# Optimization experiments

Measured on AMD Instinct MI355X. Metric: run time of the kernel, lower is better.

The kernel has to match this reference:

```python
import jax, jax.numpy as jnp
from jax import lax
import numpy as np

N, F_IN, D_MODEL = 8192, 128, 256
D_INNER, D_STATE, D_CONV, DT_RANK = 512, 16, 4, 16  # expand=2, d_state=16, d_conv=4, dt_rank=ceil(256/16)
BN_EPS = 1e-5


def setup_inputs() -> dict:
    key = jax.random.key(0)
    ks = jax.random.split(key, 12)
    rn = lambda k, s, sc: jax.random.normal(k, s, jnp.float32) * sc
    x = rn(ks[0], (N, F_IN), 1.0)
    # normalized dense adjacency (row sums ~1)
    adj = jax.random.uniform(ks[1], (N, N), jnp.float32) * (2.0 / N)
    w_gcn = rn(ks[2], (F_IN, D_MODEL), 1.0 / np.sqrt(F_IN))
    b_gcn = rn(ks[3], (D_MODEL,), 0.02)
    bn_gamma = jnp.ones((D_MODEL,), jnp.float32)
    bn_beta = jnp.zeros((D_MODEL,), jnp.float32)
    w_in = rn(ks[4], (2 * D_INNER, D_MODEL), 1.0 / np.sqrt(D_MODEL))
    conv_w = rn(ks[5], (D_INNER, D_CONV), 1.0 / np.sqrt(D_CONV))
    conv_b = rn(ks[6], (D_INNER,), 0.02)
    w_xproj = rn(ks[7], (DT_RANK + 2 * D_STATE, D_INNER), 1.0 / np.sqrt(D_INNER))
    w_dt = rn(ks[8], (D_INNER, DT_RANK), 1.0 / np.sqrt(DT_RANK))
    b_dt = rn(ks[9], (D_INNER,), 0.1)
    A_log = jnp.log(jnp.broadcast_to(jnp.arange(1, D_STATE + 1, dtype=jnp.float32), (D_INNER, D_STATE)))
    D_skip = jnp.ones((D_INNER,), jnp.float32)
    w_out = rn(ks[10], (D_MODEL, D_INNER), 1.0 / np.sqrt(D_INNER))
    return dict(x=x, adj=adj, w_gcn=w_gcn, b_gcn=b_gcn, bn_gamma=bn_gamma, bn_beta=bn_beta,
                w_in=w_in, conv_w=conv_w, conv_b=conv_b, w_xproj=w_xproj, w_dt=w_dt,
                b_dt=b_dt, A_log=A_log, D_skip=D_skip, w_out=w_out)


def _forward(x, adj, w_gcn, b_gcn, bn_gamma, bn_beta, w_in, conv_w, conv_b,
             w_xproj, w_dt, b_dt, A_log, D_skip, w_out):
    # --- GCN layer: adj @ (x @ W) + b ---
    h = adj @ (x @ w_gcn) + b_gcn            # (N, D_MODEL)
    h = jax.nn.relu(h)
    # dropout: eval mode -> identity
    # --- BatchNorm1d (batch statistics, biased var, as torch training norm) ---
    mean = jnp.mean(h, axis=0)
    var = jnp.var(h, axis=0)
    h = (h - mean) * lax.rsqrt(var + BN_EPS) * bn_gamma + bn_beta  # (N, D_MODEL)

    # --- Mamba block, batch=1, seq_len=N ---
    xz = h @ w_in.T                          # (N, 2*D_INNER)
    xm, z = jnp.split(xz, 2, axis=-1)        # (N, D_INNER) each

    # causal depthwise conv1d (kernel D_CONV) + SiLU
    xp = jnp.pad(xm, ((D_CONV - 1, 0), (0, 0)))
    xc = conv_b + sum(xp[i:i + N] * conv_w[:, i] for i in range(D_CONV))  # (N, D_INNER)
    xc = jax.nn.silu(xc)

    # input-dependent SSM parameters
    x_dbl = xc @ w_xproj.T                   # (N, DT_RANK + 2*D_STATE)
    dt_r = x_dbl[:, :DT_RANK]
    B = x_dbl[:, DT_RANK:DT_RANK + D_STATE]  # (N, D_STATE)
    C = x_dbl[:, DT_RANK + D_STATE:]         # (N, D_STATE)
    dt = jax.nn.softplus(dt_r @ w_dt.T + b_dt)  # (N, D_INNER)

    A = -jnp.exp(A_log)                      # (D_INNER, D_STATE)
    deltaA = jnp.exp(dt[:, :, None] * A[None])                 # (N, D_INNER, D_STATE)
    deltaBu = dt[:, :, None] * B[:, None, :] * xc[:, :, None]  # (N, D_INNER, D_STATE)

    def step(hs, inp):
        dA, dBu, c = inp
        hs = dA * hs + dBu                   # (D_INNER, D_STATE)
        return hs, hs @ c                    # emit (D_INNER,)

    h0 = jnp.zeros((D_INNER, D_STATE), xc.dtype)
    _, ys = lax.scan(step, h0, (deltaA, deltaBu, C))  # ys: (N, D_INNER)

    y = ys + D_skip * xc
    y = y * jax.nn.silu(z)
    out_m = y @ w_out.T                      # (N, D_MODEL)
    return out_m + h                         # residual


def reference(x, adj, w_gcn, b_gcn, bn_gamma, bn_beta, w_in, conv_w, conv_b,
              w_xproj, w_dt, b_dt, A_log, D_skip, w_out):
    return _forward(x, adj, w_gcn, b_gcn, bn_gamma, bn_beta, w_in, conv_w, conv_b,
                    w_xproj, w_dt, b_dt, A_log, D_skip, w_out)
```

## Files before the change

kernel.cpp:

```cpp
#include <hip/hip_runtime.h>
#include <stdint.h>

#define NN   8192
#define FIN  128
#define DM   256
#define DI   512
#define DST  16
#define NC   256
#define CL   32

typedef short bf16x8 __attribute__((ext_vector_type(8)));
typedef float f32x4 __attribute__((ext_vector_type(4)));
union FragU { unsigned u[4]; uint4 u4; bf16x8 v; };

__device__ __forceinline__ unsigned short f2bf(float x){
  unsigned u = __float_as_uint(x);
  return (unsigned short)((u + 0x7FFFu + ((u >> 16) & 1u)) >> 16);
}
__device__ __forceinline__ unsigned pack2(float a, float b){
  return (unsigned)f2bf(a) | ((unsigned)f2bf(b) << 16);
}
__device__ __forceinline__ unsigned pack2rn(float a, float b){
  unsigned ua = __float_as_uint(a) + 0x8000u;
  unsigned ub = __float_as_uint(b) + 0x8000u;
  return __builtin_amdgcn_perm(ub, ua, 0x07060302u);
}
__device__ __forceinline__ float bf2f(unsigned short u){
  return __uint_as_float(((unsigned)u) << 16);
}
__device__ __forceinline__ float sigmoidf_(float x){ return 1.f / (1.f + __expf(-x)); }
__device__ __forceinline__ f32x4 zero4(){ f32x4 z; z[0]=0.f; z[1]=0.f; z[2]=0.f; z[3]=0.f; return z; }

#define ASYNC16(g, l) __builtin_amdgcn_global_load_lds( \
    (const __attribute__((address_space(1))) void*)(g), \
    (__attribute__((address_space(3))) void*)(l), 16, 0, 0)
#define WAITVM3  asm volatile("s_waitcnt vmcnt(3)" ::: "memory")
#define WAITVM0  asm volatile("s_waitcnt vmcnt(0)" ::: "memory")
#define WAITLGKM0 asm volatile("s_waitcnt lgkmcnt(0)" ::: "memory")
#define BARRIER  asm volatile("s_barrier" ::: "memory")

constexpr size_t OFF_XWT   = 0;
constexpr size_t OFF_HP    = OFF_XWT   + (size_t)DM*NN*2;
constexpr size_t OFF_HB    = OFF_HP    + (size_t)2*NN*DM*4;
constexpr size_t OFF_HBNB  = OFF_HB    + (size_t)NN*DM*2;
constexpr size_t OFF_WINB  = OFF_HBNB  + (size_t)NN*DM*2;
constexpr size_t OFF_WXPB  = OFF_WINB  + (size_t)1024*256*2;
constexpr size_t OFF_WOUTB = OFF_WXPB  + (size_t)48*512*2;
constexpr size_t OFF_XMB   = OFF_WOUTB + (size_t)256*512*2;
constexpr size_t OFF_ZB    = OFF_XMB   + (size_t)NN*DI*2;
constexpr size_t OFF_XC    = OFF_ZB    + (size_t)NN*DI*2;
constexpr size_t OFF_XCB   = OFF_XC    + (size_t)NN*DI*4;
constexpr size_t OFF_XDBL  = OFF_XCB   + (size_t)NN*DI*2;
constexpr size_t OFF_DT    = OFF_XDBL  + (size_t)NN*48*4;
constexpr size_t OFF_PF    = OFF_DT    + (size_t)NN*DI*4;
constexpr size_t OFF_CY    = OFF_PF    + (size_t)NC*DI*DST*8;
constexpr size_t OFF_YB    = OFF_CY    + (size_t)NC*DI*DST*4;
constexpr size_t OFF_BNS   = OFF_YB    + (size_t)NN*DI*2;
constexpr size_t OFF_BNS2  = OFF_BNS   + 256*4;
constexpr size_t WS_NEED   = OFF_BNS2  + 256*4;

__global__ __launch_bounds__(256) void prep_kernel(
    const float* __restrict__ w_in, const float* __restrict__ w_xp, const float* __restrict__ w_out,
    unsigned short* __restrict__ o_in, unsigned short* __restrict__ o_xp, unsigned short* __restrict__ o_out)
{
  int i = blockIdx.x * 256 + threadIdx.x;
  if (i < 1024*256) o_in[i]  = f2bf(w_in[i]);
  if (i < 48*512)   o_xp[i]  = f2bf(w_xp[i]);
  if (i < 256*512)  o_out[i] = f2bf(w_out[i]);
}

__global__ __launch_bounds__(256) void gemm1_kernel(
    const float* __restrict__ x, const float* __restrict__ w, unsigned short* __restrict__ xwT)
{
  __shared__ float xs[16*128];
  const int t = threadIdx.x;
  const int m0 = blockIdx.x * 16;
  {
    int r = t >> 4, c0 = (t & 15) * 8;
    const float* src = x + (size_t)(m0 + r)*FIN + c0;
    *(float4*)&xs[r*128 + c0]     = *(const float4*)src;
    *(float4*)&xs[r*128 + c0 + 4] = *(const float4*)(src + 4);
  }
  __syncthreads();
  const int n = t;
  float acc[16];
  #pragma unroll
  for (int m = 0; m < 16; ++m) acc[m] = 0.f;
  for (int k = 0; k < 128; k += 4){
    float w0 = w[(size_t)k*DM + n];
    float w1 = w[(size_t)(k+1)*DM + n];
    float w2 = w[(size_t)(k+2)*DM + n];
    float w3 = w[(size_t)(k+3)*DM + n];
    #pragma unroll
    for (int m = 0; m < 16; ++m){
      float4 xv = *(const float4*)&xs[m*128 + k];
      acc[m] = fmaf(xv.x, w0, acc[m]);
      acc[m] = fmaf(xv.y, w1, acc[m]);
      acc[m] = fmaf(xv.z, w2, acc[m]);
      acc[m] = fmaf(xv.w, w3, acc[m]);
    }
  }
  unsigned outp[8];
  #pragma unroll
  for (int m = 0; m < 8; ++m) outp[m] = pack2(acc[2*m], acc[2*m+1]);
  unsigned short* dst = xwT + (size_t)n*NN + m0;
  ((uint4*)dst)[0] = *(uint4*)&outp[0];
  ((uint4*)dst)[1] = *(uint4*)&outp[4];
}

__global__ __launch_bounds__(512) void gemm2_kernel(
    const float* __restrict__ adj, const unsigned short* __restrict__ xwT,
    float* __restrict__ hp)
{
  __shared__ char lds[2][24576];
  const int t = threadIdx.x;
  const int wave = t >> 6, lane = t & 63, r = lane & 15, q = lane >> 4;
  const int mt = (int)blockIdx.x & 127, ks = (int)blockIdx.x >> 7;
  const int m0 = mt * 64;
  const int kb = ks * 4096;
  const int wm = wave & 1, wn = wave >> 1;

  const int arow = t >> 3;
  const int asg  = (t & 7) ^ (arow & 7);
  const float* asrc = adj + (size_t)(m0 + arow)*NN + kb + asg*4;
  const int adst = t * 16;
  const int bn0 = t >> 2;
  const int bs0 = (t & 3) ^ ((bn0 >> 1) & 3);
  const int bn1 = (512 + t) >> 2;
  const int bs1 = ((512 + t) & 3) ^ ((bn1 >> 1) & 3);
  const unsigned short* bsrc0 = xwT + (size_t)bn0*NN + kb + bs0*8;
  const unsigned short* bsrc1 = xwT + (size_t)bn1*NN + kb + bs1*8;
  const int bdst0 = 8192 + t*16;
  const int bdst1 = 8192 + (512 + t)*16;

  f32x4 acc[2][4];
  #pragma unroll
  for (int mi = 0; mi < 2; ++mi)
    #pragma unroll
    for (int ni = 0; ni < 4; ++ni) acc[mi][ni] = zero4();

  ASYNC16(asrc,       lds[0] + adst);
  ASYNC16(bsrc0,      lds[0] + bdst0);
  ASYNC16(bsrc1,      lds[0] + bdst1);
  ASYNC16(asrc + 32,  lds[1] + adst);
  ASYNC16(bsrc0 + 32, lds[1] + bdst0);
  ASYNC16(bsrc1 + 32, lds[1] + bdst1);

  const int ar0 = wm*32 + r;
  const int ar1 = ar0 + 16;
  const int aoff00 = ar0*32 + (((2*q)   ^ (ar0 & 7)) << 2);
  const int aoff01 = ar0*32 + (((2*q+1) ^ (ar0 & 7)) << 2);
  const int aoff10 = ar1*32 + (((2*q)   ^ (ar1 & 7)) << 2);
  const int aoff11 = ar1*32 + (((2*q+1) ^ (ar1 & 7)) << 2);
  int boff[4];
  #pragma unroll
  for (int ni = 0; ni < 4; ++ni){
    int nl = wn*64 + ni*16 + r;
    boff[ni] = nl*4 + (q ^ ((nl >> 1) & 3));
  }

  #pragma unroll 2
  for (int k = 0; k < 128; ++k){
    if (k < 127) { WAITVM3; } else { WAITVM0; }
    BARRIER;
    const float* Af = (const float*)lds[k & 1];
    const uint4* Bf = (const uint4*)(lds[k & 1] + 8192);
    float4 p00 = *(const float4*)(Af + aoff00);
    float4 p01 = *(const float4*)(Af + aoff01);
    float4 p10 = *(const float4*)(Af + aoff10);
    float4 p11 = *(const float4*)(Af + aoff11);
    FragU fb[4];
    #pragma unroll
    for (int ni = 0; ni < 4; ++ni) fb[ni].u4 = Bf[boff[ni]];
    WAITLGKM0;
    BARRIER;
    if (k + 2 < 128){
      int k0 = (k + 2) * 32;
      char* L = lds[k & 1];
      ASYNC16(asrc + k0,  L + adst);
      ASYNC16(bsrc0 + k0, L + bdst0);
      ASYNC16(bsrc1 + k0, L + bdst1);
    }
    FragU fa0, fa1;
    fa0.u[0] = pack2rn(p00.x, p00.y); fa0.u[1] = pack2rn(p00.z, p00.w);
    fa0.u[2] = pack2rn(p01.x, p01.y); fa0.u[3] = pack2rn(p01.z, p01.w);
    fa1.u[0] = pack2rn(p10.x, p10.y); fa1.u[1] = pack2rn(p10.z, p10.w);
    fa1.u[2] = pack2rn(p11.x, p11.y); fa1.u[3] = pack2rn(p11.z, p11.w);
    #pragma unroll
    for (int ni = 0; ni < 4; ++ni){
      acc[0][ni] = __builtin_amdgcn_mfma_f32_16x16x32_bf16(fa0.v, fb[ni].v, acc[0][ni], 0, 0, 0);
      acc[1][ni] = __builtin_amdgcn_mfma_f32_16x16x32_bf16(fa1.v, fb[ni].v, acc[1][ni], 0, 0, 0);
    }
  }

  float* hpo = hp + (size_t)ks * ((size_t)NN * DM);
  #pragma unroll
  for (int mi = 0; mi < 2; ++mi)
    #pragma unroll
    for (int ni = 0; ni < 4; ++ni){
      const int n = wn*64 + ni*16 + r;
      #pragma unroll
      for (int jr = 0; jr < 4; ++jr){
        const int m = m0 + wm*32 + mi*16 + q*4 + jr;
        hpo[(size_t)m*DM + n] = acc[mi][ni][jr];
      }
    }
}

__global__ __launch_bounds__(256) void hred_kernel(
    const float* __restrict__ hp, const float* __restrict__ b_gcn,
    unsigned short* __restrict__ hb, float* __restrict__ bns, float* __restrict__ bns2)
{
  const int c = threadIdx.x;
  const int m0 = blockIdx.x * 32;
  const float bias = b_gcn[c];
  float s1 = 0.f, s2 = 0.f;
  #pragma unroll 8
  for (int rr = 0; rr < 32; ++rr){
    size_t idx = (size_t)(m0 + rr)*DM + c;
    float v = hp[idx] + hp[(size_t)NN*DM + idx] + bias;
    v = fmaxf(v, 0.f);
    hb[idx] = f2bf(v);
    s1 += v; s2 += v*v;
  }
  atomicAdd(bns + c, s1);
  atomicAdd(bns2 + c, s2);
}

__global__ __launch_bounds__(256) void bnapply_kernel(
    const unsigned short* __restrict__ hb, const float* __restrict__ s1, const float* __restrict__ s2,
    const float* __restrict__ gamma, const float* __restrict__ beta,
    unsigned short* __restrict__ hbnb)
{
  int base = (blockIdx.x*256 + threadIdx.x) * 2;
  int c0 = base & (DM - 1);
  ushort2 hv = *(const ushort2*)(hb + base);
  float mA = s1[c0] * (1.f/NN),   mB = s1[c0+1] * (1.f/NN);
  float vA = s2[c0] * (1.f/NN) - mA*mA, vB = s2[c0+1] * (1.f/NN) - mB*mB;
  float iA = rsqrtf(vA + 1e-5f), iB = rsqrtf(vB + 1e-5f);
  float a = (bf2f(hv.x) - mA)*iA*gamma[c0]   + beta[c0];
  float b = (bf2f(hv.y) - mB)*iB*gamma[c0+1] + beta[c0+1];
  ushort2 o; o.x = f2bf(a); o.y = f2bf(b);
  *(ushort2*)(hbnb + base) = o;
}

__global__ __launch_bounds__(256) void gemm3_kernel(
    const unsigned short* __restrict__ Ab, const unsigned short* __restrict__ Wb,
    unsigned short* __restrict__ xmb, unsigned short* __restrict__ zb)
{
  __shared__ uint4 alds[2048];
  const int t = threadIdx.x;
  const int wave = t >> 6, lane = t & 63, r = lane & 15, q = lane >> 4;
  const int mb = ((int)blockIdx.x & 127) * 64;
  const int nb = ((int)blockIdx.x >> 7) * 128;
  const int wm = wave & 1, wn = wave >> 1;

  #pragma unroll
  for (int j = 0; j < 8; ++j){
    int si = j*256 + t;
    int row = si >> 5, dg = si & 31;
    int sg = dg ^ (row & 31);
    ASYNC16(Ab + (size_t)(mb + row)*DM + sg*8, (char*)alds + si*16);
  }
  __syncthreads();

  f32x4 acc[2][4];
  #pragma unroll
  for (int mi = 0; mi < 2; ++mi)
    #pragma unroll
    for (int ni = 0; ni < 4; ++ni) acc[mi][ni] = zero4();

  const unsigned short* bp[4];
  #pragma unroll
  for (int ni = 0; ni < 4; ++ni)
    bp[ni] = Wb + (size_t)(nb + wn*64 + ni*16 + r)*DM + q*8;
  FragU fb[4];
  #pragma unroll
  for (int ni = 0; ni < 4; ++ni) fb[ni].u4 = *(const uint4*)bp[ni];

  #pragma unroll
  for (int it = 0; it < 8; ++it){
    FragU fbn[4];
    if (it < 7){
      #pragma unroll
      for (int ni = 0; ni < 4; ++ni) fbn[ni].u4 = *(const uint4*)(bp[ni] + (it+1)*32);
    }
    FragU fa[2];
    #pragma unroll
    for (int mi = 0; mi < 2; ++mi){
      int row = wm*32 + mi*16 + r;
      int g = it*4 + q;
      fa[mi].u4 = alds[row*32 + (g ^ (row & 31))];
    }
    #pragma unroll
    for (int mi = 0; mi < 2; ++mi)
      #pragma unroll
      for (int ni = 0; ni < 4; ++ni)
        acc[mi][ni] = __builtin_amdgcn_mfma_f32_16x16x32_bf16(fa[mi].v, fb[ni].v, acc[mi][ni], 0, 0, 0);
    if (it < 7){
      #pragma unroll
      for (int ni = 0; ni < 4; ++ni) fb[ni] = fbn[ni];
    }
  }
  #pragma unroll
  for (int mi = 0; mi < 2; ++mi)
    #pragma unroll
    for (int ni = 0; ni < 4; ++ni){
      int nc = nb + wn*64 + ni*16 + r;
      unsigned short* dst = (nc < 512) ? (xmb + nc) : (zb + (nc - 512));
      #pragma unroll
      for (int jr = 0; jr < 4; ++jr){
        int m = mb + wm*32 + mi*16 + q*4 + jr;
        dst[(size_t)m*DI] = f2bf(acc[mi][ni][jr]);
      }
    }
}

__global__ __launch_bounds__(256) void conv_kernel(
    const unsigned short* __restrict__ xmb, const float* __restrict__ conv_w, const float* __restrict__ conv_b,
    float* __restrict__ xc, unsigned short* __restrict__ xcb)
{
  const int d0 = threadIdx.x * 2;
  const int n0 = blockIdx.x * 32;
  float4 wa = *(const float4*)(conv_w + (size_t)d0*4);
  float4 wb = *(const float4*)(conv_w + (size_t)d0*4 + 4);
  float2 bias = *(const float2*)(conv_b + d0);
  float x0a=0.f,x1a=0.f,x2a=0.f, x0b=0.f,x1b=0.f,x2b=0.f;
  #pragma unroll
  for (int j = 0; j < 3; ++j){
    int n = n0 - 3 + j;
    float va = 0.f, vb = 0.f;
    if (n >= 0){
      ushort2 u = *(const ushort2*)(xmb + (size_t)n*DI + d0);
      va = bf2f(u.x); vb = bf2f(u.y);
    }
    if (j == 0){ x0a = va; x0b = vb; }
    else if (j == 1){ x1a = va; x1b = vb; }
    else { x2a = va; x2b = vb; }
  }
  for (int j = 0; j < 32; ++j){
    int n = n0 + j;
    ushort2 u = *(const ushort2*)(xmb + (size_t)n*DI + d0);
    float x3a = bf2f(u.x), x3b = bf2f(u.y);
    float sa = bias.x + wa.x*x0a + wa.y*x1a + wa.z*x2a + wa.w*x3a;
    float sb = bias.y + wb.x*x0b + wb.y*x1b + wb.z*x2b + wb.w*x3b;
    float va = sa * sigmoidf_(sa);
    float vb = sb * sigmoidf_(sb);
    *(float2*)(xc + (size_t)n*DI + d0) = make_float2(va, vb);
    ushort2 o; o.x = f2bf(va); o.y = f2bf(vb);
    *(ushort2*)(xcb + (size_t)n*DI + d0) = o;
    x0a=x1a; x1a=x2a; x2a=x3a;
    x0b=x1b; x1b=x2b; x2b=x3b;
  }
}

__global__ __launch_bounds__(256) void gemm4_kernel(
    const unsigned short* __restrict__ Ab, const unsigned short* __restrict__ Wb, float* __restrict__ xdbl)
{
  __shared__ uint4 alds[2048];
  const int t = threadIdx.x;
  const int wave = t >> 6, lane = t & 63, r = lane & 15, q = lane >> 4;
  const int m0 = (int)blockIdx.x * 32;
  #pragma unroll
  for (int j = 0; j < 8; ++j){
    int si = j*256 + t;
    int row = si >> 6, dg = si & 63;
    int sg = dg ^ (row & 31);
    ASYNC16(Ab + (size_t)(m0 + row)*DI + sg*8, (char*)alds + si*16);
  }
  __syncthreads();
  f32x4 acc[2][3];
  #pragma unroll
  for (int mi = 0; mi < 2; ++mi)
    #pragma unroll
    for (int ni = 0; ni < 3; ++ni) acc[mi][ni] = zero4();
  const int kq = wave * 128;
  const unsigned short* bp[3];
  #pragma unroll
  for (int ni = 0; ni < 3; ++ni) bp[ni] = Wb + (size_t)(ni*16 + r)*DI + kq + q*8;
  FragU fb[3];
  #pragma unroll
  for (int ni = 0; ni < 3; ++ni) fb[ni].u4 = *(const uint4*)bp[ni];
  #pragma unroll
  for (int it = 0; it < 4; ++it){
    FragU fbn[3];
    if (it < 3){
      #pragma unroll
      for (int ni = 0; ni < 3; ++ni) fbn[ni].u4 = *(const uint4*)(bp[ni] + (it+1)*32);
    }
    FragU fa[2];
    #pragma unroll
    for (int mi = 0; mi < 2; ++mi){
      int row = mi*16 + r;
      int g = (kq >> 3) + it*4 + q;
      fa[mi].u4 = alds[row*64 + (g ^ (row & 31))];
    }
    #pragma unroll
    for (int mi = 0; mi < 2; ++mi)
      #pragma unroll
      for (int ni = 0; ni < 3; ++ni)
        acc[mi][ni] = __builtin_amdgcn_mfma_f32_16x16x32_bf16(fa[mi].v, fb[ni].v, acc[mi][ni], 0, 0, 0);
    if (it < 3){
      #pragma unroll
      for (int ni = 0; ni < 3; ++ni) fb[ni] = fbn[ni];
    }
  }
  __syncthreads();
  float* red = (float*)alds;
  if (wave > 0){
    int base = ((wave - 1)*64 + lane)*24;
    #pragma unroll
    for (int mi = 0; mi < 2; ++mi)
      #pragma unroll
      for (int ni = 0; ni < 3; ++ni)
        #pragma unroll
        for (int jr = 0; jr < 4; ++jr)
          red[base + (mi*3 + ni)*4 + jr] = acc[mi][ni][jr];
  }
  __syncthreads();
  if (wave == 0){
    #pragma unroll
    for (int w = 0; w < 3; ++w){
      int base = (w*64 + lane)*24;
      #pragma unroll
      for (int mi = 0; mi < 2; ++mi)
        #pragma unroll
        for (int ni = 0; ni < 3; ++ni)
          #pragma unroll
          for (int jr = 0; jr < 4; ++jr)
            acc[mi][ni][jr] += red[base + (mi*3 + ni)*4 + jr];
    }
    #pragma unroll
    for (int mi = 0; mi < 2; ++mi)
      #pragma unroll
      for (int ni = 0; ni < 3; ++ni)
        #pragma unroll
        for (int jr = 0; jr < 4; ++jr)
          xdbl[(size_t)(m0 + mi*16 + q*4 + jr)*48 + ni*16 + r] = acc[mi][ni][jr];
  }
}

__global__ __launch_bounds__(256) void dt_kernel(
    const float* __restrict__ xdbl, const float* __restrict__ w_dt, const float* __restrict__ b_dt,
    float* __restrict__ dt)
{
  __shared__ float xr[64*16];
  const int t = threadIdx.x;
  const int dg = (int)blockIdx.x & 1;
  const int n0 = ((int)blockIdx.x >> 1) * 64;
  const int d = dg*256 + t;
  #pragma unroll
  for (int j = 0; j < 4; ++j){
    int idx = t + 256*j;
    xr[idx] = xdbl[(size_t)(n0 + (idx >> 4))*48 + (idx & 15)];
  }
  __syncthreads();
  const float4* wp = (const float4*)(w_dt + (size_t)d*16);
  float4 w0 = wp[0], w1 = wp[1], w2 = wp[2], w3 = wp[3];
  float bias = b_dt[d];
  for (int j = 0; j < 64; ++j){
    const float4* xp = (const float4*)(xr + j*16);
    float4 a0 = xp[0], a1 = xp[1], a2 = xp[2], a3 = xp[3];
    float a = bias;
    a += w0.x*a0.x + w0.y*a0.y + w0.z*a0.z + w0.w*a0.w;
    a += w1.x*a1.x + w1.y*a1.y + w1.z*a1.z + w1.w*a1.w;
    a += w2.x*a2.x + w2.y*a2.y + w2.z*a2.z + w2.w*a2.w;
    a += w3.x*a3.x + w3.y*a3.y + w3.z*a3.z + w3.w*a3.w;
    float o = (a > 20.f) ? a : log1pf(__expf(a));
    dt[(size_t)(n0 + j)*DI + d] = o;
  }
}

__global__ __launch_bounds__(256) void scanA_kernel(
    const float* __restrict__ dt, const float* __restrict__ xc,
    const float* __restrict__ xdbl, const float* __restrict__ A_log,
    float2* __restrict__ PF)
{
  __shared__ float Bs[CL*DST];
  const int t = threadIdx.x;
  const int c = (int)blockIdx.x >> 1;
  const int d = (((int)blockIdx.x & 1) << 8) + t;
  #pragma unroll
  for (int j = 0; j < 2; ++j){
    int idx = t + 256*j;
    Bs[idx] = xdbl[(size_t)(c*CL + (idx >> 4))*48 + 16 + (idx & 15)];
  }
  __syncthreads();
  float Av[DST], hs[DST];
  {
    const float4* Ap = (const float4*)(A_log + (size_t)d*DST);
    #pragma unroll
    for (int s4 = 0; s4 < 4; ++s4){
      float4 a4 = Ap[s4];
      Av[s4*4+0] = -__expf(a4.x); Av[s4*4+1] = -__expf(a4.y);
      Av[s4*4+2] = -__expf(a4.z); Av[s4*4+3] = -__expf(a4.w);
    }
  }
  #pragma unroll
  for (int s = 0; s < DST; ++s) hs[s] = 0.f;
  float sdt = 0.f;
  const size_t rb = (size_t)c*CL*DI + d;
  float dtv = dt[rb], xcv = xc[rb];
  for (int tt = 0; tt < CL; ++tt){
    float dtn = 0.f, xcn = 0.f;
    if (tt + 1 < CL){
      dtn = dt[rb + (size_t)(tt+1)*DI];
      xcn = xc[rb + (size_t)(tt+1)*DI];
    }
    float u = dtv * xcv;
    sdt += dtv;
    float bv[DST];
    *(float4*)&bv[0]  = *(const float4*)&Bs[tt*16];
    *(float4*)&bv[4]  = *(const float4*)&Bs[tt*16 + 4];
    *(float4*)&bv[8]  = *(const float4*)&Bs[tt*16 + 8];
    *(float4*)&bv[12] = *(const float4*)&Bs[tt*16 + 12];
    #pragma unroll
    for (int s = 0; s < DST; ++s)
      hs[s] = __expf(dtv * Av[s]) * hs[s] + u * bv[s];
    dtv = dtn; xcv = xcn;
  }
  float4* out = (float4*)(PF + (size_t)c*(DI*DST) + (size_t)d*DST);
  #pragma unroll
  for (int j = 0; j < 8; ++j){
    float4 v;
    v.x = __expf(Av[2*j] * sdt);   v.y = hs[2*j];
    v.z = __expf(Av[2*j+1] * sdt); v.w = hs[2*j+1];
    out[j] = v;
  }
}

__global__ __launch_bounds__(128) void scanB_kernel(
    const float2* __restrict__ PF, float* __restrict__ Cy)
{
  const int ds = (int)blockIdx.x*128 + (int)threadIdx.x;
  float2 A0[16], A1[16];
  #pragma unroll
  for (int j = 0; j < 16; ++j) A0[j] = PF[(size_t)j*8192 + ds];
  #pragma unroll
  for (int j = 0; j < 16; ++j) A1[j] = PF[(size_t)(16 + j)*8192 + ds];
  float cy = 0.f;
  Cy[ds] = 0.f;
  #pragma unroll
  for (int g = 0; g < 16; ++g){
    #pragma unroll
    for (int j = 0; j < 16; ++j){
      int i = g*16 + j;
      if (i < NC - 1){
        float2 pf = (g & 1) ? A1[j] : A0[j];
        cy = pf.x * cy + pf.y;
        Cy[(size_t)(i + 1)*8192 + ds] = cy;
      }
    }
    int gn = g + 2;
    if (gn < 16){
      #pragma unroll
      for (int j = 0; j < 16; ++j){
        float2 v = PF[(size_t)(gn*16 + j)*8192 + ds];
        if (g & 1) A1[j] = v; else A0[j] = v;
      }
    }
  }
}

__global__ __launch_bounds__(256) void scanC_kernel(
    const float* __restrict__ dt, const float* __restrict__ xc,
    const float* __restrict__ xdbl, const float* __restrict__ A_log,
    const float* __restrict__ Cy, const float* __restrict__ Dskip,
    const unsigned short* __restrict__ zb, unsigned short* __restrict__ yb)
{
  __shared__ float Bs[CL*DST];
  __shared__ float Cs[CL*DST];
  const int t = threadIdx.x;
  const int c = (int)blockIdx.x >> 1;
  const int d = (((int)blockIdx.x & 1) << 8) + t;
  #pragma unroll
  for (int j = 0; j < 2; ++j){
    int idx = t + 256*j;
    int tg = c*CL + (idx >> 4);
    Bs[idx] = xdbl[(size_t)tg*48 + 16 + (idx & 15)];
    Cs[idx] = xdbl[(size_t)tg*48 + 32 + (idx & 15)];
  }
  __syncthreads();
  float Av[DST], hs[DST];
  {
    const float4* Ap = (const float4*)(A_log + (size_t)d*DST);
    #pragma unroll
    for (int s4 = 0; s4 < 4; ++s4){
      float4 a4 = Ap[s4];
      Av[s4*4+0] = -__expf(a4.x); Av[s4*4+1] = -__expf(a4.y);
      Av[s4*4+2] = -__expf(a4.z); Av[s4*4+3] = -__expf(a4.w);
    }
  }
  {
    const float4* hp4 = (const float4*)(Cy + (size_t)c*(DI*DST) + (size_t)d*DST);
    #pragma unroll
    for (int s4 = 0; s4 < 4; ++s4){
      float4 h4 = hp4[s4];
      hs[s4*4+0] = h4.x; hs[s4*4+1] = h4.y; hs[s4*4+2] = h4.z; hs[s4*4+3] = h4.w;
    }
  }
  const float Dv = Dskip[d];
  const size_t rb = (size_t)c*CL*DI + d;
  float dtv = dt[rb], xcv = xc[rb];
  unsigned short zv0 = zb[rb];
  for (int tt = 0; tt < CL; ++tt){
    float dtn = 0.f, xcn = 0.f;
    unsigned short zn = 0;
    if (tt + 1 < CL){
      dtn = dt[rb + (size_t)(tt+1)*DI];
      xcn = xc[rb + (size_t)(tt+1)*DI];
      zn  = zb[rb + (size_t)(tt+1)*DI];
    }
    float u = dtv * xcv;
    float bv[DST], cv[DST];
    *(float4*)&bv[0]  = *(const float4*)&Bs[tt*16];
    *(float4*)&bv[4]  = *(const float4*)&Bs[tt*16 + 4];
    *(float4*)&bv[8]  = *(const float4*)&Bs[tt*16 + 8];
    *(float4*)&bv[12] = *(const float4*)&Bs[tt*16 + 12];
    *(float4*)&cv[0]  = *(const float4*)&Cs[tt*16];
    *(float4*)&cv[4]  = *(const float4*)&Cs[tt*16 + 4];
    *(float4*)&cv[8]  = *(const float4*)&Cs[tt*16 + 8];
    *(float4*)&cv[12] = *(const float4*)&Cs[tt*16 + 12];
    float y0 = 0.f, y1 = 0.f;
    #pragma unroll
    for (int s = 0; s < DST; s += 2){
      hs[s]   = __expf(dtv * Av[s])   * hs[s]   + u * bv[s];
      hs[s+1] = __expf(dtv * Av[s+1]) * hs[s+1] + u * bv[s+1];
      y0 += hs[s]   * cv[s];
      y1 += hs[s+1] * cv[s+1];
    }
    float z = bf2f(zv0);
    float yf = ((y0 + y1) + Dv * xcv) * (z * sigmoidf_(z));
    yb[rb + (size_t)tt*DI] = f2bf(yf);
    dtv = dtn; xcv = xcn; zv0 = zn;
  }
}

__global__ __launch_bounds__(512) void gemm5_kernel(
    const unsigned short* __restrict__ yb, const unsigned short* __restrict__ Wb,
    const unsigned short* __restrict__ hbnb, float* __restrict__ out)
{
  __shared__ uint4 alds[2048];
  const int t = threadIdx.x;
  const int wave = t >> 6, lane = t & 63, r = lane & 15, q = lane >> 4;
  const int m0 = (int)blockIdx.x * 32;
  #pragma unroll
  for (int j = 0; j < 4; ++j){
    int si = j*512 + t;
    int row = si >> 6, dg = si & 63;
    int sg = dg ^ (row & 31);
    ASYNC16(yb + (size_t)(m0 + row)*DI + sg*8, (char*)alds + si*16);
  }
  __syncthreads();
  f32x4 acc[2][2];
  #pragma unroll
  for (int mi = 0; mi < 2; ++mi)
    #pragma unroll
    for (int ni = 0; ni < 2; ++ni) acc[mi][ni] = zero4();
  const int nw = wave * 32;
  const unsigned short* bp0 = Wb + (size_t)(nw + r)*DI + q*8;
  const unsigned short* bp1 = Wb + (size_t)(nw + 16 + r)*DI + q*8;
  FragU fb0, fb1;
  fb0.u4 = *(const uint4*)bp0;
  fb1.u4 = *(const uint4*)bp1;
  #pragma unroll
  for (int it = 0; it < 16; ++it){
    FragU fn0, fn1;
    if (it < 15){
      fn0.u4 = *(const uint4*)(bp0 + (it+1)*32);
      fn1.u4 = *(const uint4*)(bp1 + (it+1)*32);
    }
    FragU fa[2];
    #pragma unroll
    for (int mi = 0; mi < 2; ++mi){
      int row = mi*16 + r;
      int g = it*4 + q;
      fa[mi].u4 = alds[row*64 + (g ^ (row & 31))];
    }
    acc[0][0] = __builtin_amdgcn_mfma_f32_16x16x32_bf16(fa[0].v, fb0.v, acc[0][0], 0, 0, 0);
    acc[0][1] = __builtin_amdgcn_mfma_f32_16x16x32_bf16(fa[0].v, fb1.v, acc[0][1], 0, 0, 0);
    acc[1][0] = __builtin_amdgcn_mfma_f32_16x16x32_bf16(fa[1].v, fb0.v, acc[1][0], 0, 0, 0);
    acc[1][1] = __builtin_amdgcn_mfma_f32_16x16x32_bf16(fa[1].v, fb1.v, acc[1][1], 0, 0, 0);
    if (it < 15){ fb0 = fn0; fb1 = fn1; }
  }
  #pragma unroll
  for (int mi = 0; mi < 2; ++mi)
    #pragma unroll
    for (int ni = 0; ni < 2; ++ni){
      const int n = nw + ni*16 + r;
      #pragma unroll
      for (int jr = 0; jr < 4; ++jr){
        const int m = m0 + mi*16 + q*4 + jr;
        size_t idx = (size_t)m*DM + n;
        out[idx] = acc[mi][ni][jr] + bf2f(hbnb[idx]);
      }
    }
}

extern "C" void kernel_launch(void* const* d_in, const int* in_sizes, int n_in,
                              void* d_out, int out_size, void* d_ws, size_t ws_size,
                              hipStream_t stream)
{
  const float* x      = (const float*)d_in[0];
  const float* adj    = (const float*)d_in[1];
  const float* w_gcn  = (const float*)d_in[2];
  const float* b_gcn  = (const float*)d_in[3];
  const float* gamma  = (const float*)d_in[4];
  const float* beta   = (const float*)d_in[5];
  const float* w_in   = (const float*)d_in[6];
  const float* conv_w = (const float*)d_in[7];
  const float* conv_b = (const float*)d_in[8];
  const float* w_xp   = (const float*)d_in[9];
  const float* w_dt   = (const float*)d_in[10];
  const float* b_dt   = (const float*)d_in[11];
  const float* A_log  = (const float*)d_in[12];
  const float* D_skip = (const float*)d_in[13];
  const float* w_out  = (const float*)d_in[14];
  float* out = (float*)d_out;
  char* ws = (char*)d_ws;
  if (ws_size < WS_NEED) return;

  unsigned short* xwT   = (unsigned short*)(ws + OFF_XWT);
  float*          hp    = (float*)(ws + OFF_HP);
  unsigned short* hb    = (unsigned short*)(ws + OFF_HB);
  unsigned short* hbnb  = (unsigned short*)(ws + OFF_HBNB);
  unsigned short* winb  = (unsigned short*)(ws + OFF_WINB);
  unsigned short* wxpb  = (unsigned short*)(ws + OFF_WXPB);
  unsigned short* woutb = (unsigned short*)(ws + OFF_WOUTB);
  unsigned short* xmb   = (unsigned short*)(ws + OFF_XMB);
  unsigned short* zb    = (unsigned short*)(ws + OFF_ZB);
  float*          xc    = (float*)(ws + OFF_XC);
  unsigned short* xcb   = (unsigned short*)(ws + OFF_XCB);
  float*          xdbl  = (float*)(ws + OFF_XDBL);
  float*          dtb   = (float*)(ws + OFF_DT);
  float2*         PF    = (float2*)(ws + OFF_PF);
  float*          Cy    = (float*)(ws + OFF_CY);
  unsigned short* yb    = (unsigned short*)(ws + OFF_YB);
  float*          bns   = (float*)(ws + OFF_BNS);
  float*          bns2  = (float*)(ws + OFF_BNS2);

  hipMemsetAsync(bns, 0, 2*256*sizeof(float), stream);

  prep_kernel   <<<1024, 256, 0, stream>>>(w_in, w_xp, w_out, winb, wxpb, woutb);
  gemm1_kernel  <<<512,  256, 0, stream>>>(x, w_gcn, xwT);
  gemm2_kernel  <<<256,  512, 0, stream>>>(adj, xwT, hp);
  hred_kernel   <<<256,  256, 0, stream>>>(hp, b_gcn, hb, bns, bns2);
  bnapply_kernel<<<4096, 256, 0, stream>>>(hb, bns, bns2, gamma, beta, hbnb);
  gemm3_kernel  <<<1024, 256, 0, stream>>>(hbnb, winb, xmb, zb);
  conv_kernel   <<<256,  256, 0, stream>>>(xmb, conv_w, conv_b, xc, xcb);
  gemm4_kernel  <<<256,  256, 0, stream>>>(xcb, wxpb, xdbl);
  dt_kernel     <<<256,  256, 0, stream>>>(xdbl, w_dt, b_dt, dtb);
  scanA_kernel  <<<512,  256, 0, stream>>>(dtb, xc, xdbl, A_log, PF);
  scanB_kernel  <<<64,   128, 0, stream>>>(PF, Cy);
  scanC_kernel  <<<512,  256, 0, stream>>>(dtb, xc, xdbl, A_log, Cy, D_skip, zb, yb);
  gemm5_kernel  <<<256,  512, 0, stream>>>(yb, woutb, hbnb, out);
}
```

Measured before the change: 629.8 us.

## Enlarge adjacency GEMM tile to 128 rows with triple-buffered LDS pipeline

Doubles the M tile of the adj@xW GEMM from 64 to 128 rows per block. To keep the block count the same, split-K goes from 2 to 4 ways. The LDS pipeline moves from double to triple buffering with dynamic shared memory, so loads are issued three stages ahead. Each wave now computes 4x4 MFMA tiles, which reuses each B fragment across twice as many A rows. The partial-sum buffer is aliased onto the later PF scratch region, and the reduction kernel now sums four partials. The intent is to raise arithmetic intensity and latency hiding in the dominant GEMM. The cost is more registers, extra partial-sum traffic, and one block per CU.

New measurement: 598.0 us. -5.0%, faster.

```diff
diff --git a/kernel.cpp b/kernel.cpp
--- a/kernel.cpp
+++ b/kernel.cpp
@@ -34,14 +34,15 @@
 #define ASYNC16(g, l) __builtin_amdgcn_global_load_lds( \
     (const __attribute__((address_space(1))) void*)(g), \
     (__attribute__((address_space(3))) void*)(l), 16, 0, 0)
+#define WAITVM8  asm volatile("s_waitcnt vmcnt(8)" ::: "memory")
+#define WAITVM4  asm volatile("s_waitcnt vmcnt(4)" ::: "memory")
 #define WAITVM3  asm volatile("s_waitcnt vmcnt(3)" ::: "memory")
 #define WAITVM0  asm volatile("s_waitcnt vmcnt(0)" ::: "memory")
 #define WAITLGKM0 asm volatile("s_waitcnt lgkmcnt(0)" ::: "memory")
 #define BARRIER  asm volatile("s_barrier" ::: "memory")
 
 constexpr size_t OFF_XWT   = 0;
-constexpr size_t OFF_HP    = OFF_XWT   + (size_t)DM*NN*2;
-constexpr size_t OFF_HB    = OFF_HP    + (size_t)2*NN*DM*4;
+constexpr size_t OFF_HB    = OFF_XWT   + (size_t)DM*NN*2;
 constexpr size_t OFF_HBNB  = OFF_HB    + (size_t)NN*DM*2;
 constexpr size_t OFF_WINB  = OFF_HBNB  + (size_t)NN*DM*2;
 constexpr size_t OFF_WXPB  = OFF_WINB  + (size_t)1024*256*2;
@@ -58,6 +59,7 @@
 constexpr size_t OFF_BNS   = OFF_YB    + (size_t)NN*DI*2;
 constexpr size_t OFF_BNS2  = OFF_BNS   + 256*4;
 constexpr size_t WS_NEED   = OFF_BNS2  + 256*4;
+constexpr size_t OFF_HP    = OFF_PF;
 
 __global__ __launch_bounds__(256) void prep_kernel(
     const float* __restrict__ w_in, const float* __restrict__ w_xp, const float* __restrict__ w_out,
@@ -108,100 +110,104 @@
   ((uint4*)dst)[1] = *(uint4*)&outp[4];
 }
 
-__global__ __launch_bounds__(512) void gemm2_kernel(
+__global__ __launch_bounds__(512, 1) void gemm2_kernel(
     const float* __restrict__ adj, const unsigned short* __restrict__ xwT,
     float* __restrict__ hp)
 {
-  __shared__ char lds[2][24576];
+  extern __shared__ char lds[];
   const int t = threadIdx.x;
   const int wave = t >> 6, lane = t & 63, r = lane & 15, q = lane >> 4;
-  const int mt = (int)blockIdx.x & 127, ks = (int)blockIdx.x >> 7;
-  const int m0 = mt * 64;
-  const int kb = ks * 4096;
+  const int mt = (int)blockIdx.x >> 2, ks = (int)blockIdx.x & 3;
+  const int m0 = mt * 128;
+  const int kb = ks * 2048;
   const int wm = wave & 1, wn = wave >> 1;
 
-  const int arow = t >> 3;
-  const int asg  = (t & 7) ^ (arow & 7);
-  const float* asrc = adj + (size_t)(m0 + arow)*NN + kb + asg*4;
-  const int adst = t * 16;
-  const int bn0 = t >> 2;
-  const int bs0 = (t & 3) ^ ((bn0 >> 1) & 3);
-  const int bn1 = (512 + t) >> 2;
-  const int bs1 = ((512 + t) & 3) ^ ((bn1 >> 1) & 3);
-  const unsigned short* bsrc0 = xwT + (size_t)bn0*NN + kb + bs0*8;
-  const unsigned short* bsrc1 = xwT + (size_t)bn1*NN + kb + bs1*8;
-  const int bdst0 = 8192 + t*16;
-  const int bdst1 = 8192 + (512 + t)*16;
-
-  f32x4 acc[2][4];
-  #pragma unroll
-  for (int mi = 0; mi < 2; ++mi)
+  const int arow = t >> 3, ag = t & 7;
+  const float* asrcA = adj + (size_t)(m0 + arow)*NN + kb + ((ag ^ (arow & 7)) << 2);
+  const float* asrcB = asrcA + (size_t)64*NN;
+  const int bnl = t >> 2, bg = t & 3;
+  const unsigned short* bsrcA = xwT + (size_t)bnl*NN + kb + ((bg ^ ((bnl >> 1) & 3)) << 3);
+  const unsigned short* bsrcB = bsrcA + (size_t)128*NN;
+  const int dA0 = t*16, dA1 = 8192 + t*16, dB0 = 16384 + t*16, dB1 = 24576 + t*16;
+
+  f32x4 acc[4][4];
+  #pragma unroll
+  for (int mi = 0; mi < 4; ++mi)
     #pragma unroll
     for (int ni = 0; ni < 4; ++ni) acc[mi][ni] = zero4();
 
-  ASYNC16(asrc,       lds[0] + adst);
-  ASYNC16(bsrc0,      lds[0] + bdst0);
-  ASYNC16(bsrc1,      lds[0] + bdst1);
-  ASYNC16(asrc + 32,  lds[1] + adst);
-  ASYNC16(bsrc0 + 32, lds[1] + bdst0);
-  ASYNC16(bsrc1 + 32, lds[1] + bdst1);
-
-  const int ar0 = wm*32 + r;
-  const int ar1 = ar0 + 16;
-  const int aoff00 = ar0*32 + (((2*q)   ^ (ar0 & 7)) << 2);
-  const int aoff01 = ar0*32 + (((2*q+1) ^ (ar0 & 7)) << 2);
-  const int aoff10 = ar1*32 + (((2*q)   ^ (ar1 & 7)) << 2);
-  const int aoff11 = ar1*32 + (((2*q+1) ^ (ar1 & 7)) << 2);
-  int boff[4];
+  #pragma unroll
+  for (int s = 0; s < 3; ++s){
+    char* L = lds + s*32768;
+    ASYNC16(asrcA + s*32, L + dA0);
+    ASYNC16(asrcB + s*32, L + dA1);
+    ASYNC16(bsrcA + s*32, L + dB0);
+    ASYNC16(bsrcB + s*32, L + dB1);
+  }
+
+  int aoff[4][2], boff[4];
+  #pragma unroll
+  for (int mi = 0; mi < 4; ++mi){
+    int row = wm*64 + mi*16 + r;
+    aoff[mi][0] = row*32 + (((2*q)   ^ (row & 7)) << 2);
+    aoff[mi][1] = row*32 + (((2*q+1) ^ (row & 7)) << 2);
+  }
   #pragma unroll
   for (int ni = 0; ni < 4; ++ni){
     int nl = wn*64 + ni*16 + r;
     boff[ni] = nl*4 + (q ^ ((nl >> 1) & 3));
   }
 
-  #pragma unroll 2
-  for (int k = 0; k < 128; ++k){
-    if (k < 127) { WAITVM3; } else { WAITVM0; }
+  int rb = 0;
+  for (int k = 0; k < 64; ++k){
+    if (k < 62) { WAITVM8; } else if (k == 62) { WAITVM4; } else { WAITVM0; }
     BARRIER;
-    const float* Af = (const float*)lds[k & 1];
-    const uint4* Bf = (const uint4*)(lds[k & 1] + 8192);
-    float4 p00 = *(const float4*)(Af + aoff00);
-    float4 p01 = *(const float4*)(Af + aoff01);
-    float4 p10 = *(const float4*)(Af + aoff10);
-    float4 p11 = *(const float4*)(Af + aoff11);
+    char* Lb = lds + rb*32768;
+    const float* Af = (const float*)Lb;
+    const uint4* Bf = (const uint4*)(Lb + 16384);
+    float4 pa[4][2];
     FragU fb[4];
+    #pragma unroll
+    for (int mi = 0; mi < 4; ++mi){
+      pa[mi][0] = *(const float4*)(Af + aoff[mi][0]);
+      pa[mi][1] = *(const float4*)(Af + aoff[mi][1]);
+    }
     #pragma unroll
     for (int ni = 0; ni < 4; ++ni) fb[ni].u4 = Bf[boff[ni]];
     WAITLGKM0;
     BARRIER;
-    if (k + 2 < 128){
-      int k0 = (k + 2) * 32;
-      char* L = lds[k & 1];
-      ASYNC16(asrc + k0,  L + adst);
-      ASYNC16(bsrc0 + k0, L + bdst0);
-      ASYNC16(bsrc1 + k0, L + bdst1);
-    }
-    FragU fa0, fa1;
-    fa0.u[0] = pack2rn(p00.x, p00.y); fa0.u[1] = pack2rn(p00.z, p00.w);
-    fa0.u[2] = pack2rn(p01.x, p01.y); fa0.u[3] = pack2rn(p01.z, p01.w);
-    fa1.u[0] = pack2rn(p10.x, p10.y); fa1.u[1] = pack2rn(p10.z, p10.w);
-    fa1.u[2] = pack2rn(p11.x, p11.y); fa1.u[3] = pack2rn(p11.z, p11.w);
-    #pragma unroll
-    for (int ni = 0; ni < 4; ++ni){
-      acc[0][ni] = __builtin_amdgcn_mfma_f32_16x16x32_bf16(fa0.v, fb[ni].v, acc[0][ni], 0, 0, 0);
-      acc[1][ni] = __builtin_amdgcn_mfma_f32_16x16x32_bf16(fa1.v, fb[ni].v, acc[1][ni], 0, 0, 0);
-    }
+    if (k < 61){
+      int ko = (k + 3) * 32;
+      ASYNC16(asrcA + ko, Lb + dA0);
+      ASYNC16(asrcB + ko, Lb + dA1);
+      ASYNC16(bsrcA + ko, Lb + dB0);
+      ASYNC16(bsrcB + ko, Lb + dB1);
+    }
+    FragU fa[4];
+    #pragma unroll
+    for (int mi = 0; mi < 4; ++mi){
+      fa[mi].u[0] = pack2rn(pa[mi][0].x, pa[mi][0].y);
+      fa[mi].u[1] = pack2rn(pa[mi][0].z, pa[mi][0].w);
+      fa[mi].u[2] = pack2rn(pa[mi][1].x, pa[mi][1].y);
+      fa[mi].u[3] = pack2rn(pa[mi][1].z, pa[mi][1].w);
+    }
+    #pragma unroll
+    for (int mi = 0; mi < 4; ++mi)
+      #pragma unroll
+      for (int ni = 0; ni < 4; ++ni)
+        acc[mi][ni] = __builtin_amdgcn_mfma_f32_16x16x32_bf16(fa[mi].v, fb[ni].v, acc[mi][ni], 0, 0, 0);
+    rb = (rb == 2) ? 0 : rb + 1;
   }
 
   float* hpo = hp + (size_t)ks * ((size_t)NN * DM);
   #pragma unroll
-  for (int mi = 0; mi < 2; ++mi)
+  for (int mi = 0; mi < 4; ++mi)
     #pragma unroll
     for (int ni = 0; ni < 4; ++ni){
       const int n = wn*64 + ni*16 + r;
       #pragma unroll
       for (int jr = 0; jr < 4; ++jr){
-        const int m = m0 + wm*32 + mi*16 + q*4 + jr;
+        const int m = m0 + wm*64 + mi*16 + q*4 + jr;
         hpo[(size_t)m*DM + n] = acc[mi][ni][jr];
       }
     }
@@ -211,6 +217,7 @@
     const float* __restrict__ hp, const float* __restrict__ b_gcn,
     unsigned short* __restrict__ hb, float* __restrict__ bns, float* __restrict__ bns2)
 {
+  const size_t NND = (size_t)NN * DM;
   const int c = threadIdx.x;
   const int m0 = blockIdx.x * 32;
   const float bias = b_gcn[c];
@@ -218,7 +225,7 @@
   #pragma unroll 8
   for (int rr = 0; rr < 32; ++rr){
     size_t idx = (size_t)(m0 + rr)*DM + c;
-    float v = hp[idx] + hp[(size_t)NN*DM + idx] + bias;
+    float v = hp[idx] + hp[NND + idx] + hp[2*NND + idx] + hp[3*NND + idx] + bias;
     v = fmaxf(v, 0.f);
     hb[idx] = f2bf(v);
     s1 += v; s2 += v*v;
@@ -741,9 +748,12 @@
 
   hipMemsetAsync(bns, 0, 2*256*sizeof(float), stream);
 
+  hipFuncSetAttribute((const void*)gemm2_kernel,
+                      hipFuncAttributeMaxDynamicSharedMemorySize, 98304);
+
   prep_kernel   <<<1024, 256, 0, stream>>>(w_in, w_xp, w_out, winb, wxpb, woutb);
   gemm1_kernel  <<<512,  256, 0, stream>>>(x, w_gcn, xwT);
-  gemm2_kernel  <<<256,  512, 0, stream>>>(adj, xwT, hp);
+  gemm2_kernel  <<<256,  512, 98304, stream>>>(adj, xwT, hp);
   hred_kernel   <<<256,  256, 0, stream>>>(hp, b_gcn, hb, bns, bns2);
   bnapply_kernel<<<4096, 256, 0, stream>>>(hb, bns, bns2, gamma, beta, hbnb);
   gemm3_kernel  <<<1024, 256, 0, stream>>>(hbnb, winb, xmb, zb);
```
